# Kernel tuning notes

Hardware: AMD Instinct MI355X
Metric: run time of the kernel (lower is better)

The kernel has to match this reference:

```python
import jax, jax.numpy as jnp
import numpy as np

B, S = 64, 1024
D_INPUT, D_POLAR, N_LAYERS, KAN, N_CLASSES = 256, 256, 8, 32, 1000
PI = float(np.pi)
EPS = 1e-8


def _gelu(v):
    return jax.nn.gelu(v, approximate=False)  # torch nn.GELU default = exact erf


def setup_inputs() -> dict:
    key = jax.random.key(0)
    ks = jax.random.split(key, 16)

    def rn(k, shape, fan_in):
        return jax.random.normal(k, shape, jnp.float32) / np.sqrt(fan_in)

    return {
        "x": jax.random.normal(ks[0], (B, S, D_INPUT), jnp.float32),
        "embed_w": rn(ks[1], (D_INPUT, 2 * D_POLAR), D_INPUT),
        "embed_b": jnp.zeros((2 * D_POLAR,), jnp.float32),
        "mag_w1": rn(ks[2], (N_LAYERS, 1, KAN), 1),
        "mag_b1": jnp.zeros((N_LAYERS, KAN), jnp.float32),
        "mag_w2": rn(ks[3], (N_LAYERS, KAN, 1), KAN),
        "mag_b2": jnp.zeros((N_LAYERS, 1), jnp.float32),
        "ph_w1": rn(ks[4], (N_LAYERS, 2, KAN), 2),
        "ph_b1": jnp.zeros((N_LAYERS, KAN), jnp.float32),
        "ph_w2": rn(ks[5], (N_LAYERS, KAN, 2), KAN),
        "ph_b2": jnp.zeros((N_LAYERS, 2), jnp.float32),
        "cls_w1": rn(ks[6], (D_POLAR, KAN), D_POLAR),
        "cls_b1": jnp.zeros((KAN,), jnp.float32),
        "cls_w2": rn(ks[7], (KAN, N_CLASSES), KAN),
        "cls_b2": jnp.zeros((N_CLASSES,), jnp.float32),
    }


def _forward(x, embed_w, embed_b, mag_w1, mag_b1, mag_w2, mag_b2,
             ph_w1, ph_b1, ph_w2, ph_b2, cls_w1, cls_b1, cls_w2, cls_b2):
    h = x @ embed_w + embed_b                      # [B,S,2D]
    r = jnp.abs(h[..., :D_POLAR]) + 0.1            # [B,S,D]
    theta = h[..., D_POLAR:] * PI                  # [B,S,D]
    for i in range(N_LAYERS):
        xc = r * jnp.cos(theta)
        yc = r * jnp.sin(theta)
        xm = xc.mean(axis=1, keepdims=True)        # [B,1,D]
        ym = yc.mean(axis=1, keepdims=True)
        r_agg = jnp.sqrt(xm * xm + ym * ym + EPS)
        th_agg = jnp.arctan2(ym, xm)
        # magnitude MLP (1 -> 32 -> 1) in log space, per channel
        log_r = jnp.log(r_agg + EPS)[..., None]    # [B,1,D,1]
        lr = _gelu(log_r @ mag_w1[i] + mag_b1[i]) @ mag_w2[i] + mag_b2[i]
        r_trans = jnp.exp(lr[..., 0])              # [B,1,D]
        # phase MLP (2 -> 32 -> 2) on (sin, cos)
        pin = jnp.stack([jnp.sin(th_agg), jnp.cos(th_agg)], axis=-1)  # [B,1,D,2]
        pout = _gelu(pin @ ph_w1[i] + ph_b1[i]) @ ph_w2[i] + ph_b2[i]
        norm = jnp.sqrt(pout[..., 0] ** 2 + pout[..., 1] ** 2 + EPS)
        th_trans = jnp.arctan2(pout[..., 0] / norm, pout[..., 1] / norm)
        x_out = xc + r_trans * jnp.cos(th_trans)
        y_out = yc + r_trans * jnp.sin(th_trans)
        r = jnp.sqrt(x_out * x_out + y_out * y_out + EPS)
        theta = jnp.arctan2(y_out, x_out)
    pooled = r.mean(axis=1)                        # [B,D]
    return _gelu(pooled @ cls_w1 + cls_b1) @ cls_w2 + cls_b2  # [B,n_classes]


def reference(x, embed_w, embed_b, mag_w1, mag_b1, mag_w2, mag_b2,
              ph_w1, ph_b1, ph_w2, ph_b2, cls_w1, cls_b1, cls_w2, cls_b2):
    return _forward(x, embed_w, embed_b, mag_w1, mag_b1, mag_w2, mag_b2,
                    ph_w1, ph_b1, ph_w2, ph_b2, cls_w1, cls_b1, cls_w2, cls_b2)
```

## Files before the change

kernel.cpp:

```cpp
#include <hip/hip_runtime.h>
#include <hip/hip_bf16.h>
#include <hip/hip_fp16.h>

#define EPS 1e-8f
#define PI_F 3.14159265358979323846f

typedef _Float16 half8 __attribute__((ext_vector_type(8)));
typedef _Float16 half4 __attribute__((ext_vector_type(4)));
typedef float f32x4 __attribute__((ext_vector_type(4)));

__device__ __forceinline__ float gelu_exact(float v) {
    return 0.5f * v * (1.0f + erff(v * 0.70710678118654752f));
}

__global__ void convertW(const float* __restrict__ W,
                         _Float16* __restrict__ Wth, _Float16* __restrict__ Wtl) {
    int idx = blockIdx.x * 256 + threadIdx.x;
    int col = idx & 511, k = idx >> 9;
    int d = col & 255, g = d >> 6;
    int j = g * 128 + ((col < 256) ? (d & 63) : (64 + (d & 63)));
    float f = W[k * 512 + col];
    _Float16 h = (_Float16)f;
    Wth[j * 256 + k] = h;
    Wtl[j * 256 + k] = (_Float16)(f - (float)h);
}

__global__ __launch_bounds__(256, 3) void gemm_embed(
    const float* __restrict__ x,
    const _Float16* __restrict__ Wth, const _Float16* __restrict__ Wtl,
    const float* __restrict__ bias,
    _Float16* __restrict__ XY,
    float* __restrict__ XMsum, float* __restrict__ YMsum)
{
    __shared__ __attribute__((aligned(16))) _Float16 Ah[4096], Al[4096], Bh[4096], Bl[4096];
    const int tid  = threadIdx.x;
    const int wave = tid >> 6;
    const int lane = tid & 63;
    const int g    = blockIdx.x;
    const int m0   = blockIdx.y * 128;
    const int q    = lane >> 4, ln = lane & 15;

    f32x4 acc[8][2];
#pragma unroll
    for (int mi = 0; mi < 8; ++mi) {
        acc[mi][0] = (f32x4){0.f, 0.f, 0.f, 0.f};
        acc[mi][1] = (f32x4){0.f, 0.f, 0.f, 0.f};
    }

    for (int kt = 0; kt < 8; ++kt) {
        __syncthreads();
#pragma unroll
        for (int c2 = 0; c2 < 2; ++c2) {
            int idx = c2 * 256 + tid;
            int r = idx >> 2, c = idx & 3;
            size_t go = (size_t)(g * 128 + r) * 256 + kt * 32 + c * 8;
            half8 vh = *(const half8*)(Wth + go);
            half8 vl = *(const half8*)(Wtl + go);
            int pos = c ^ ((r >> 1) & 3);
            *(half8*)&Bh[r * 32 + pos * 8] = vh;
            *(half8*)&Bl[r * 32 + pos * 8] = vl;
        }
#pragma unroll
        for (int L = 0; L < 2; ++L) {
            int idx = L * 256 + tid;
            int r = idx >> 2, cq = idx & 3;
            const float* src = x + (size_t)(m0 + r) * 256 + kt * 32 + cq * 8;
            const float4 f0 = *(const float4*)(src);
            const float4 f1 = *(const float4*)(src + 4);
            half8 hh, ll;
            hh[0] = (_Float16)f0.x; ll[0] = (_Float16)(f0.x - (float)hh[0]);
            hh[1] = (_Float16)f0.y; ll[1] = (_Float16)(f0.y - (float)hh[1]);
            hh[2] = (_Float16)f0.z; ll[2] = (_Float16)(f0.z - (float)hh[2]);
            hh[3] = (_Float16)f0.w; ll[3] = (_Float16)(f0.w - (float)hh[3]);
            hh[4] = (_Float16)f1.x; ll[4] = (_Float16)(f1.x - (float)hh[4]);
            hh[5] = (_Float16)f1.y; ll[5] = (_Float16)(f1.y - (float)hh[5]);
            hh[6] = (_Float16)f1.z; ll[6] = (_Float16)(f1.z - (float)hh[6]);
            hh[7] = (_Float16)f1.w; ll[7] = (_Float16)(f1.w - (float)hh[7]);
            int pos = cq ^ ((r >> 1) & 3);
            *(half8*)&Ah[r * 32 + pos * 8] = hh;
            *(half8*)&Al[r * 32 + pos * 8] = ll;
        }
        __syncthreads();

        half8 bh[2], bl[2];
#pragma unroll
        for (int t = 0; t < 2; ++t) {
            int rn = (t * 4 + wave) * 16 + ln;
            int off = rn * 32 + (q ^ ((rn >> 1) & 3)) * 8;
            bh[t] = *(const half8*)&Bh[off];
            bl[t] = *(const half8*)&Bl[off];
        }
#pragma unroll
        for (int mi = 0; mi < 8; ++mi) {
            int row = mi * 16 + ln;
            int off = row * 32 + (q ^ ((row >> 1) & 3)) * 8;
            half8 am = *(const half8*)&Ah[off];
            half8 alm = *(const half8*)&Al[off];
#pragma unroll
            for (int t = 0; t < 2; ++t) {
                acc[mi][t] = __builtin_amdgcn_mfma_f32_16x16x32_f16(am,  bh[t], acc[mi][t], 0, 0, 0);
                acc[mi][t] = __builtin_amdgcn_mfma_f32_16x16x32_f16(am,  bl[t], acc[mi][t], 0, 0, 0);
                acc[mi][t] = __builtin_amdgcn_mfma_f32_16x16x32_f16(alm, bh[t], acc[mi][t], 0, 0, 0);
            }
        }
    }

    const int d  = g * 64 + wave * 16 + ln;
    const int b  = m0 >> 10;
    const float b1 = bias[d];
    const float b2 = bias[256 + d];
    float sx = 0.f, sy = 0.f;
    union { _Float16 h[2]; unsigned u; } pk;
#pragma unroll
    for (int mi = 0; mi < 8; ++mi) {
#pragma unroll
        for (int i = 0; i < 4; ++i) {
            const int row = m0 + mi * 16 + q * 4 + i;
            const float h1 = acc[mi][0][i] + b1;
            const float h2 = acc[mi][1][i] + b2;
            const float rr = fabsf(h1) + 0.1f;
            float sv, cv;
            __sincosf(PI_F * h2, &sv, &cv);
            const float xc = rr * cv, yc = rr * sv;
            pk.h[0] = (_Float16)xc; pk.h[1] = (_Float16)yc;
            *(unsigned*)(XY + (size_t)row * 512 + d * 2) = pk.u;
            sx += xc; sy += yc;
        }
    }
    sx += __shfl_down(sx, 32); sx += __shfl_down(sx, 16);
    sy += __shfl_down(sy, 32); sy += __shfl_down(sy, 16);
    if (lane < 16) {
        atomicAdd(&XMsum[b * 256 + d], sx);
        atomicAdd(&YMsum[b * 256 + d], sy);
    }
}

__global__ __launch_bounds__(256) void layers_kernel(
    const float* __restrict__ XMsum, const float* __restrict__ YMsum,
    const float* __restrict__ mw1, const float* __restrict__ mb1,
    const float* __restrict__ mw2, const float* __restrict__ mb2,
    const float* __restrict__ pw1, const float* __restrict__ pb1,
    const float* __restrict__ pw2, const float* __restrict__ pb2,
    float* __restrict__ DX, float* __restrict__ DY)
{
    __shared__ float s_mw1[256], s_mb1[256], s_mw2[256], s_mb2[8];
    __shared__ float s_pw1[512], s_pb1[256], s_pw2[512], s_pb2[16];
    const int tid = threadIdx.x;
    s_mw1[tid] = mw1[tid]; s_mb1[tid] = mb1[tid];
    s_mw2[tid] = mw2[tid]; s_pb1[tid] = pb1[tid];
    s_pw1[tid] = pw1[tid]; s_pw1[256 + tid] = pw1[256 + tid];
    s_pw2[tid] = pw2[tid]; s_pw2[256 + tid] = pw2[256 + tid];
    if (tid < 8)  s_mb2[tid] = mb2[tid];
    if (tid < 16) s_pb2[tid] = pb2[tid];
    __syncthreads();

    const int gid = blockIdx.x * 256 + tid;
    const int idx = gid >> 3;
    const int sub = gid & 7;
    float xm = XMsum[idx] * (1.0f / 1024.0f);
    float ym = YMsum[idx] * (1.0f / 1024.0f);
    float dxa = 0.f, dya = 0.f;
#pragma unroll 1
    for (int i = 0; i < 8; ++i) {
        float r2    = xm * xm + ym * ym;
        float r_agg = sqrtf(r2 + EPS);
        float hyp   = sqrtf(r2);
        float inv   = hyp > 0.f ? 1.0f / hyp : 0.f;
        float st    = ym * inv;
        float ct    = hyp > 0.f ? xm * inv : 1.0f;
        float log_r = logf(r_agg + EPS);
        float lr = 0.f, p0 = 0.f, p1 = 0.f;
#pragma unroll
        for (int k4 = 0; k4 < 4; ++k4) {
            int k = sub * 4 + k4;
            float hm = gelu_exact(log_r * s_mw1[i * 32 + k] + s_mb1[i * 32 + k]);
            lr += hm * s_mw2[i * 32 + k];
            float hp = gelu_exact(st * s_pw1[i * 64 + k] + ct * s_pw1[i * 64 + 32 + k] + s_pb1[i * 32 + k]);
            p0 += hp * s_pw2[i * 64 + 2 * k + 0];
            p1 += hp * s_pw2[i * 64 + 2 * k + 1];
        }
        lr += __shfl_xor(lr, 1); lr += __shfl_xor(lr, 2); lr += __shfl_xor(lr, 4);
        p0 += __shfl_xor(p0, 1); p0 += __shfl_xor(p0, 2); p0 += __shfl_xor(p0, 4);
        p1 += __shfl_xor(p1, 1); p1 += __shfl_xor(p1, 2); p1 += __shfl_xor(p1, 4);
        lr += s_mb2[i];
        p0 += s_pb2[i * 2 + 0];
        p1 += s_pb2[i * 2 + 1];
        float r_trans = expf(lr);
        float hp2  = sqrtf(p0 * p0 + p1 * p1);
        float invp = hp2 > 0.f ? 1.0f / hp2 : 0.f;
        float ctt  = hp2 > 0.f ? p1 * invp : 1.0f;
        float stt  = p0 * invp;
        float dx = r_trans * ctt;
        float dy = r_trans * stt;
        dxa += dx; dya += dy; xm += dx; ym += dy;
    }
    if (sub == 0) { DX[idx] = dxa; DY[idx] = dya; }
}

__global__ __launch_bounds__(256) void pool_kernel(
    const _Float16* __restrict__ XY,
    const float* __restrict__ DX, const float* __restrict__ DY,
    float* __restrict__ pooled)
{
    __shared__ float red[256][4];
    const int b = blockIdx.x, sc = blockIdx.y, tid = threadIdx.x;
    const int dg = tid & 63;
    const int sh = tid >> 6;
    const int d = dg * 4;
    float dxv[4], dyv[4], s[4];
#pragma unroll
    for (int j = 0; j < 4; ++j) {
        dxv[j] = DX[b * 256 + d + j];
        dyv[j] = DY[b * 256 + d + j];
        s[j] = 0.f;
    }
    const int r0 = sc * 128 + sh * 32;
    const size_t base = ((size_t)b * 1024 + r0) * 512 + d * 2;
#pragma unroll 4
    for (int i = 0; i < 32; ++i) {
        half8 v = *(const half8*)(XY + base + (size_t)i * 512);
#pragma unroll
        for (int j = 0; j < 4; ++j) {
            float xv = (float)v[2 * j] + dxv[j];
            float yv = (float)v[2 * j + 1] + dyv[j];
            s[j] += sqrtf(xv * xv + yv * yv + EPS);
        }
    }
#pragma unroll
    for (int j = 0; j < 4; ++j) red[tid][j] = s[j];
    __syncthreads();
    if (tid < 64) {
#pragma unroll
        for (int j = 0; j < 4; ++j) {
            float t = red[tid][j] + red[tid + 64][j] + red[tid + 128][j] + red[tid + 192][j];
            atomicAdd(&pooled[b * 256 + tid * 4 + j], t);
        }
    }
}

__global__ __launch_bounds__(256) void cls_kernel(
    const float* __restrict__ pooled,
    const float* __restrict__ w1, const float* __restrict__ b1,
    const float* __restrict__ w2, const float* __restrict__ b2,
    float* __restrict__ out)
{
    __shared__ float pl[256];
    __shared__ float part[8][32];
    __shared__ float hd[32];
    const int b = blockIdx.x, tid = threadIdx.x;
    pl[tid] = pooled[b * 256 + tid] * (1.0f / 1024.0f);
    __syncthreads();
    const int hu = tid & 31, kc = tid >> 5;
    float a = 0.f;
    for (int k = kc * 32; k < kc * 32 + 32; ++k) a += pl[k] * w1[k * 32 + hu];
    part[kc][hu] = a;
    __syncthreads();
    if (tid < 32) {
        float s = b1[tid];
#pragma unroll
        for (int c = 0; c < 8; ++c) s += part[c][tid];
        hd[tid] = gelu_exact(s);
    }
    __syncthreads();
    for (int n = tid; n < 1000; n += 256) {
        float s = b2[n];
#pragma unroll
        for (int k = 0; k < 32; ++k) s += hd[k] * w2[k * 1000 + n];
        out[b * 1000 + n] = s;
    }
}

extern "C" void kernel_launch(void* const* d_in, const int* in_sizes, int n_in,
                              void* d_out, int out_size, void* d_ws, size_t ws_size,
                              hipStream_t stream)
{
    const float* x       = (const float*)d_in[0];
    const float* embed_w = (const float*)d_in[1];
    const float* embed_b = (const float*)d_in[2];
    const float* mag_w1  = (const float*)d_in[3];
    const float* mag_b1  = (const float*)d_in[4];
    const float* mag_w2  = (const float*)d_in[5];
    const float* mag_b2  = (const float*)d_in[6];
    const float* ph_w1   = (const float*)d_in[7];
    const float* ph_b1   = (const float*)d_in[8];
    const float* ph_w2   = (const float*)d_in[9];
    const float* ph_b2   = (const float*)d_in[10];
    const float* cls_w1  = (const float*)d_in[11];
    const float* cls_b1  = (const float*)d_in[12];
    const float* cls_w2  = (const float*)d_in[13];
    const float* cls_b2  = (const float*)d_in[14];
    float* out = (float*)d_out;

    char* ws = (char*)d_ws;
    _Float16* XY  = (_Float16*)(ws + 0);
    _Float16* Wth = (_Float16*)(ws + 67108864);
    _Float16* Wtl = (_Float16*)(ws + 67371008);
    float* XMsum  = (float*)(ws + 67633152);
    float* YMsum  = (float*)(ws + 67698688);
    float* pooled = (float*)(ws + 67764224);
    float* DX     = (float*)(ws + 67829760);
    float* DY     = (float*)(ws + 67895296);

    hipMemsetAsync(ws + 67633152, 0, 3 * 65536, stream);

    convertW<<<512, 256, 0, stream>>>(embed_w, Wth, Wtl);
    gemm_embed<<<dim3(4, 512), 256, 0, stream>>>(x, Wth, Wtl, embed_b, XY, XMsum, YMsum);
    layers_kernel<<<512, 256, 0, stream>>>(XMsum, YMsum, mag_w1, mag_b1, mag_w2, mag_b2,
                                           ph_w1, ph_b1, ph_w2, ph_b2, DX, DY);
    pool_kernel<<<dim3(64, 8), 256, 0, stream>>>(XY, DX, DY, pooled);
    cls_kernel<<<64, 256, 0, stream>>>(pooled, cls_w1, cls_b1, cls_w2, cls_b2, out);
}
```

Measured before the change: 216.7 us.

## Store polar intermediates in FP8, remap GEMM blocks per XCD, fold memset

The intermediate (xc,yc) buffer moves from fp16 to packed fp8, halving the bytes written by the GEMM and read by the pool kernel, and the pool kernel is rewritten to decode fp8 pairs eight channels per thread. The GEMM grid becomes 1D with an XCD-aware block remap, occupancy rises to 4 blocks, and the A fragments are loaded once so the hi/lo MFMA passes can be grouped. The workspace memset is folded into convertW. FP8 storage of the activations sharply lowers the precision of the pooled magnitudes and may break the accuracy tolerance.

```diff
diff --git a/kernel.cpp b/kernel.cpp
--- a/kernel.cpp
+++ b/kernel.cpp
@@ -8,14 +8,17 @@
 typedef _Float16 half8 __attribute__((ext_vector_type(8)));
 typedef _Float16 half4 __attribute__((ext_vector_type(4)));
 typedef float f32x4 __attribute__((ext_vector_type(4)));
+typedef float f32x2 __attribute__((ext_vector_type(2)));
 
 __device__ __forceinline__ float gelu_exact(float v) {
     return 0.5f * v * (1.0f + erff(v * 0.70710678118654752f));
 }
 
 __global__ void convertW(const float* __restrict__ W,
-                         _Float16* __restrict__ Wth, _Float16* __restrict__ Wtl) {
+                         _Float16* __restrict__ Wth, _Float16* __restrict__ Wtl,
+                         float* __restrict__ zero_base) {
     int idx = blockIdx.x * 256 + threadIdx.x;
+    if (idx < 49152) zero_base[idx] = 0.f;
     int col = idx & 511, k = idx >> 9;
     int d = col & 255, g = d >> 6;
     int j = g * 128 + ((col < 256) ? (d & 63) : (64 + (d & 63)));
@@ -25,19 +28,23 @@
     Wtl[j * 256 + k] = (_Float16)(f - (float)h);
 }
 
-__global__ __launch_bounds__(256, 3) void gemm_embed(
+__global__ __launch_bounds__(256, 4) void gemm_embed(
     const float* __restrict__ x,
     const _Float16* __restrict__ Wth, const _Float16* __restrict__ Wtl,
     const float* __restrict__ bias,
-    _Float16* __restrict__ XY,
+    unsigned short* __restrict__ XY8,
     float* __restrict__ XMsum, float* __restrict__ YMsum)
 {
     __shared__ __attribute__((aligned(16))) _Float16 Ah[4096], Al[4096], Bh[4096], Bl[4096];
     const int tid  = threadIdx.x;
     const int wave = tid >> 6;
     const int lane = tid & 63;
-    const int g    = blockIdx.x;
-    const int m0   = blockIdx.y * 128;
+    const int id   = blockIdx.x;
+    const int xcd  = id & 7;
+    const int s    = id >> 3;
+    const int g    = s & 3;
+    const int mt   = (s >> 2) * 8 + xcd;
+    const int m0   = mt * 128;
     const int q    = lane >> 4, ln = lane & 15;
 
     f32x4 acc[8][2];
@@ -82,7 +89,7 @@
         }
         __syncthreads();
 
-        half8 bh[2], bl[2];
+        half8 bh[2], bl[2], am[8];
 #pragma unroll
         for (int t = 0; t < 2; ++t) {
             int rn = (t * 4 + wave) * 16 + ln;
@@ -93,15 +100,25 @@
 #pragma unroll
         for (int mi = 0; mi < 8; ++mi) {
             int row = mi * 16 + ln;
-            int off = row * 32 + (q ^ ((row >> 1) & 3)) * 8;
-            half8 am = *(const half8*)&Ah[off];
-            half8 alm = *(const half8*)&Al[off];
-#pragma unroll
-            for (int t = 0; t < 2; ++t) {
-                acc[mi][t] = __builtin_amdgcn_mfma_f32_16x16x32_f16(am,  bh[t], acc[mi][t], 0, 0, 0);
-                acc[mi][t] = __builtin_amdgcn_mfma_f32_16x16x32_f16(am,  bl[t], acc[mi][t], 0, 0, 0);
-                acc[mi][t] = __builtin_amdgcn_mfma_f32_16x16x32_f16(alm, bh[t], acc[mi][t], 0, 0, 0);
-            }
+            am[mi] = *(const half8*)&Ah[row * 32 + (q ^ ((row >> 1) & 3)) * 8];
+        }
+#pragma unroll
+        for (int mi = 0; mi < 8; ++mi)
+#pragma unroll
+            for (int t = 0; t < 2; ++t)
+                acc[mi][t] = __builtin_amdgcn_mfma_f32_16x16x32_f16(am[mi], bh[t], acc[mi][t], 0, 0, 0);
+#pragma unroll
+        for (int mi = 0; mi < 8; ++mi)
+#pragma unroll
+            for (int t = 0; t < 2; ++t)
+                acc[mi][t] = __builtin_amdgcn_mfma_f32_16x16x32_f16(am[mi], bl[t], acc[mi][t], 0, 0, 0);
+#pragma unroll
+        for (int mi = 0; mi < 8; ++mi) {
+            int row = mi * 16 + ln;
+            half8 alv = *(const half8*)&Al[row * 32 + (q ^ ((row >> 1) & 3)) * 8];
+#pragma unroll
+            for (int t = 0; t < 2; ++t)
+                acc[mi][t] = __builtin_amdgcn_mfma_f32_16x16x32_f16(alv, bh[t], acc[mi][t], 0, 0, 0);
         }
     }
 
@@ -110,7 +127,6 @@
     const float b1 = bias[d];
     const float b2 = bias[256 + d];
     float sx = 0.f, sy = 0.f;
-    union { _Float16 h[2]; unsigned u; } pk;
 #pragma unroll
     for (int mi = 0; mi < 8; ++mi) {
 #pragma unroll
@@ -122,8 +138,8 @@
             float sv, cv;
             __sincosf(PI_F * h2, &sv, &cv);
             const float xc = rr * cv, yc = rr * sv;
-            pk.h[0] = (_Float16)xc; pk.h[1] = (_Float16)yc;
-            *(unsigned*)(XY + (size_t)row * 512 + d * 2) = pk.u;
+            int pk = __builtin_amdgcn_cvt_pk_fp8_f32(xc, yc, 0, false);
+            XY8[(size_t)row * 256 + d] = (unsigned short)pk;
             sx += xc; sy += yc;
         }
     }
@@ -198,42 +214,48 @@
 }
 
 __global__ __launch_bounds__(256) void pool_kernel(
-    const _Float16* __restrict__ XY,
+    const unsigned short* __restrict__ XY8,
     const float* __restrict__ DX, const float* __restrict__ DY,
     float* __restrict__ pooled)
 {
-    __shared__ float red[256][4];
+    __shared__ float red[256][9];
     const int b = blockIdx.x, sc = blockIdx.y, tid = threadIdx.x;
-    const int dg = tid & 63;
-    const int sh = tid >> 6;
-    const int d = dg * 4;
-    float dxv[4], dyv[4], s[4];
-#pragma unroll
-    for (int j = 0; j < 4; ++j) {
-        dxv[j] = DX[b * 256 + d + j];
-        dyv[j] = DY[b * 256 + d + j];
+    const int dg = tid & 31;
+    const int sh = tid >> 5;
+    const int d0 = dg * 8;
+    float dxv[8], dyv[8], s[8];
+#pragma unroll
+    for (int j = 0; j < 8; ++j) {
+        dxv[j] = DX[b * 256 + d0 + j];
+        dyv[j] = DY[b * 256 + d0 + j];
         s[j] = 0.f;
     }
-    const int r0 = sc * 128 + sh * 32;
-    const size_t base = ((size_t)b * 1024 + r0) * 512 + d * 2;
+    const int r0 = sc * 128 + sh * 16;
+    const size_t base = ((size_t)b * 1024 + r0) * 256 + d0;
 #pragma unroll 4
-    for (int i = 0; i < 32; ++i) {
-        half8 v = *(const half8*)(XY + base + (size_t)i * 512);
-#pragma unroll
-        for (int j = 0; j < 4; ++j) {
-            float xv = (float)v[2 * j] + dxv[j];
-            float yv = (float)v[2 * j + 1] + dyv[j];
-            s[j] += sqrtf(xv * xv + yv * yv + EPS);
-        }
-    }
-#pragma unroll
-    for (int j = 0; j < 4; ++j) red[tid][j] = s[j];
-    __syncthreads();
-    if (tid < 64) {
-#pragma unroll
-        for (int j = 0; j < 4; ++j) {
-            float t = red[tid][j] + red[tid + 64][j] + red[tid + 128][j] + red[tid + 192][j];
-            atomicAdd(&pooled[b * 256 + tid * 4 + j], t);
+    for (int i = 0; i < 16; ++i) {
+        const int4 v = *(const int4*)(XY8 + base + (size_t)i * 256);
+        const int wv[4] = {v.x, v.y, v.z, v.w};
+#pragma unroll
+        for (int w = 0; w < 4; ++w) {
+            f32x2 pa = __builtin_amdgcn_cvt_pk_f32_fp8(wv[w], false);
+            f32x2 pb = __builtin_amdgcn_cvt_pk_f32_fp8(wv[w], true);
+            float xa = pa[0] + dxv[2 * w],     ya = pa[1] + dyv[2 * w];
+            float xb = pb[0] + dxv[2 * w + 1], yb = pb[1] + dyv[2 * w + 1];
+            s[2 * w]     += sqrtf(xa * xa + ya * ya + EPS);
+            s[2 * w + 1] += sqrtf(xb * xb + yb * yb + EPS);
+        }
+    }
+#pragma unroll
+    for (int j = 0; j < 8; ++j) red[tid][j] = s[j];
+    __syncthreads();
+    if (tid < 32) {
+#pragma unroll
+        for (int j = 0; j < 8; ++j) {
+            float t = 0.f;
+#pragma unroll
+            for (int c = 0; c < 8; ++c) t += red[c * 32 + tid][j];
+            atomicAdd(&pooled[b * 256 + tid * 8 + j], t);
         }
     }
 }
@@ -292,21 +314,19 @@
     float* out = (float*)d_out;
 
     char* ws = (char*)d_ws;
-    _Float16* XY  = (_Float16*)(ws + 0);
-    _Float16* Wth = (_Float16*)(ws + 67108864);
-    _Float16* Wtl = (_Float16*)(ws + 67371008);
-    float* XMsum  = (float*)(ws + 67633152);
-    float* YMsum  = (float*)(ws + 67698688);
-    float* pooled = (float*)(ws + 67764224);
-    float* DX     = (float*)(ws + 67829760);
-    float* DY     = (float*)(ws + 67895296);
-
-    hipMemsetAsync(ws + 67633152, 0, 3 * 65536, stream);
-
-    convertW<<<512, 256, 0, stream>>>(embed_w, Wth, Wtl);
-    gemm_embed<<<dim3(4, 512), 256, 0, stream>>>(x, Wth, Wtl, embed_b, XY, XMsum, YMsum);
+    unsigned short* XY8 = (unsigned short*)(ws + 0);
+    _Float16* Wth = (_Float16*)(ws + 33554432);
+    _Float16* Wtl = (_Float16*)(ws + 33816576);
+    float* XMsum  = (float*)(ws + 34078720);
+    float* YMsum  = (float*)(ws + 34144256);
+    float* pooled = (float*)(ws + 34209792);
+    float* DX     = (float*)(ws + 34275328);
+    float* DY     = (float*)(ws + 34340864);
+
+    convertW<<<512, 256, 0, stream>>>(embed_w, Wth, Wtl, XMsum);
+    gemm_embed<<<2048, 256, 0, stream>>>(x, Wth, Wtl, embed_b, XY8, XMsum, YMsum);
     layers_kernel<<<512, 256, 0, stream>>>(XMsum, YMsum, mag_w1, mag_b1, mag_w2, mag_b2,
                                            ph_w1, ph_b1, ph_w2, ph_b2, DX, DY);
-    pool_kernel<<<dim3(64, 8), 256, 0, stream>>>(XY, DX, DY, pooled);
+    pool_kernel<<<dim3(64, 8), 256, 0, stream>>>(XY8, DX, DY, pooled);
     cls_kernel<<<64, 256, 0, stream>>>(pooled, cls_w1, cls_b1, cls_w2, cls_b2, out);
 }
```

Result: no change. 213.1 us (-1.7%).
